# Kernel tuning notes

Measured on AMD Instinct MI355X. Metric: run time of the kernel, lower is better.

## Reference

```python
import jax, jax.numpy as jnp
import numpy as np

N_NODES = 50000
N_EDGES = 800000
F_IN = 128
F_HID = 128
N_CLS = 1
E_TR = 100000
E_TE = 20000


def setup_inputs() -> dict:
    key = jax.random.key(0)
    ks = jax.random.split(key, 16)
    inp = {
        'x': jax.random.normal(ks[0], (N_NODES, F_IN), dtype=jnp.float32),
        'edge_index': jax.random.randint(ks[1], (2, N_EDGES), 0, N_NODES, dtype=jnp.int32),
        'pos_edges_train': jax.random.randint(ks[2], (2, E_TR), 0, N_NODES, dtype=jnp.int32),
        'neg_edges_train': jax.random.randint(ks[3], (2, E_TR), 0, N_NODES, dtype=jnp.int32),
        'pos_edges_test': jax.random.randint(ks[4], (2, E_TE), 0, N_NODES, dtype=jnp.int32),
        'neg_edges_test': jax.random.randint(ks[5], (2, E_TE), 0, N_NODES, dtype=jnp.int32),
    }
    s = 0.05
    inp['W0'] = jax.random.normal(ks[6], (F_IN, F_HID), dtype=jnp.float32) * s
    inp['b0'] = jnp.zeros((F_HID,), dtype=jnp.float32)
    inp['W1'] = jax.random.normal(ks[7], (F_HID, F_HID), dtype=jnp.float32) * s
    inp['b1'] = jnp.zeros((F_HID,), dtype=jnp.float32)
    inp['W2'] = jax.random.normal(ks[8], (F_HID, F_HID), dtype=jnp.float32) * s
    inp['b2'] = jnp.zeros((F_HID,), dtype=jnp.float32)
    inp['W3'] = jax.random.normal(ks[9], (F_HID, F_HID), dtype=jnp.float32) * s
    inp['b3'] = jnp.zeros((F_HID,), dtype=jnp.float32)
    inp['Wl1'] = jax.random.normal(ks[10], (2 * F_HID, F_HID), dtype=jnp.float32) * s
    inp['bl1'] = jnp.zeros((F_HID,), dtype=jnp.float32)
    inp['Wl2'] = jax.random.normal(ks[11], (F_HID, N_CLS), dtype=jnp.float32) * s
    inp['bl2'] = jnp.zeros((N_CLS,), dtype=jnp.float32)
    return inp


def _gcn_conv(h, W, b, src, dst, dis):
    # PyG GCNConv: out = D^{-1/2}(A+I)D^{-1/2} (h W) + b, with self loops folded in analytically
    hw = h @ W                                           # [N, F]
    msg = hw[src] * dis[src][:, None]                    # [E, F]
    agg = jax.ops.segment_sum(msg, dst, num_segments=N_NODES)
    return agg * dis[:, None] + hw * (dis ** 2)[:, None] + b


def _edge_feats(x, e):
    return jnp.concatenate([x[e[0]], x[e[1]]], axis=1)


def reference(x, edge_index, pos_edges_train, neg_edges_train, pos_edges_test, neg_edges_test,
              W0, b0, W1, b1, W2, b2, W3, b3, Wl1, bl1, Wl2, bl2):
    src, dst = edge_index[0], edge_index[1]
    # degree with self loop (+1), symmetric normalization
    deg = jax.ops.segment_sum(jnp.ones((src.shape[0],), jnp.float32), dst, num_segments=N_NODES) + 1.0
    dis = deg ** -0.5

    h = jax.nn.relu(_gcn_conv(x, W0, b0, src, dst, dis))
    h = jax.nn.relu(_gcn_conv(h, W1, b1, src, dst, dis))
    h = jax.nn.relu(_gcn_conv(h, W2, b2, src, dst, dis))
    h = _gcn_conv(h, W3, b3, src, dst, dis)

    x_train = jnp.concatenate([_edge_feats(h, pos_edges_train), _edge_feats(h, neg_edges_train)], axis=0)
    x_test = jnp.concatenate([_edge_feats(h, pos_edges_test), _edge_feats(h, neg_edges_test)], axis=0)
    n_train = x_train.shape[0]
    z = jnp.concatenate([x_train, x_test], axis=0)
    z = jax.nn.relu(z @ Wl1 + bl1)
    z = (z @ Wl2 + bl2).squeeze(1)
    return (z[:n_train], z[n_train:])
```

## Files before the change

kernel.cpp:

```cpp
#include <hip/hip_runtime.h>
#include <math.h>

#define NN 50000
#define NE 800000
#define FD 128
#define SCAN_B 196
#define NTR 100000
#define NTE 20000


__global__ __launch_bounds__(256) void k_zero_int(int* __restrict__ p, int n) {
    int i = blockIdx.x * 256 + threadIdx.x;
    if (i < n) p[i] = 0;
}

__global__ __launch_bounds__(256) void k_count(const int* __restrict__ dst, int* __restrict__ deg) {
    int e = blockIdx.x * 256 + threadIdx.x;
    if (e < NE) atomicAdd(&deg[dst[e]], 1);
}


__global__ __launch_bounds__(256) void k_scan1(const int* __restrict__ deg,
                                               int* __restrict__ partial,
                                               int* __restrict__ bsum,
                                               float* __restrict__ dis) {
    __shared__ int wsum[4];
    const int t = threadIdx.x, lane = t & 63, wid = t >> 6;
    const int i = blockIdx.x * 256 + t;
    int v = (i < NN) ? deg[i] : 0;
    int sc = v;
#pragma unroll
    for (int d = 1; d < 64; d <<= 1) {
        int o = __shfl_up(sc, d, 64);
        if (lane >= d) sc += o;
    }
    if (lane == 63) wsum[wid] = sc;
    __syncthreads();
    int pre = 0;
    for (int w = 0; w < wid; ++w) pre += wsum[w];
    if (i < NN) {
        partial[i] = pre + sc - v;
        dis[i] = (float)(1.0 / sqrt((double)(v + 1)));
    }
    if (t == 255) bsum[blockIdx.x] = pre + sc;
}

__global__ __launch_bounds__(256) void k_scan2(int* __restrict__ bsum) {
    __shared__ int wsum[4];
    const int t = threadIdx.x, lane = t & 63, wid = t >> 6;
    int v = (t < SCAN_B) ? bsum[t] : 0;
    int sc = v;
#pragma unroll
    for (int d = 1; d < 64; d <<= 1) {
        int o = __shfl_up(sc, d, 64);
        if (lane >= d) sc += o;
    }
    if (lane == 63) wsum[wid] = sc;
    __syncthreads();
    int pre = 0;
    for (int w = 0; w < wid; ++w) pre += wsum[w];
    if (t < SCAN_B) bsum[t] = pre + sc - v;
}

__global__ __launch_bounds__(256) void k_scan3(const int* __restrict__ partial,
                                               const int* __restrict__ bsum,
                                               int* __restrict__ offs,
                                               int* __restrict__ cursor) {
    const int i = blockIdx.x * 256 + threadIdx.x;
    if (i < NN) {
        int o = partial[i] + bsum[blockIdx.x];
        offs[i] = o;
        cursor[i] = o;
    }
    if (i == 0) offs[NN] = NE;
}


__global__ __launch_bounds__(256) void k_fill(const int* __restrict__ src, const int* __restrict__ dst,
                                              int* __restrict__ cursor, int* __restrict__ srcs_sorted) {
    int e = blockIdx.x * 256 + threadIdx.x;
    if (e < NE) {
        int d = dst[e];
        int p = atomicAdd(&cursor[d], 1);
        srcs_sorted[p] = src[e];
    }
}


__global__ __launch_bounds__(256) void k_gemm(const float* __restrict__ A,
                                              const float* __restrict__ W,
                                              const float* __restrict__ dis,
                                              float* __restrict__ C, int nrows) {
    __shared__ float As[32][128];
    const int t = threadIdx.x;
    const int row0 = blockIdx.x * 32;

    for (int idx = t; idx < 32 * 32; idx += 256) {
        int r = idx >> 5, c = idx & 31;
        float4 v = make_float4(0.f, 0.f, 0.f, 0.f);
        if (row0 + r < nrows)
            v = reinterpret_cast<const float4*>(A)[(size_t)(row0 + r) * 32 + c];
        reinterpret_cast<float4*>(&As[r][0])[c] = v;
    }
    __syncthreads();

    const int cg = t & 31;
    const int eg = t >> 5;
    float acc[4][4] = {{0.f}};

    const float4* W4 = reinterpret_cast<const float4*>(W);
    const float4* As4 = reinterpret_cast<const float4*>(As);

    float4 w0 = W4[0 * 32 + cg];
    float4 w1 = W4[1 * 32 + cg];
    float4 w2 = W4[2 * 32 + cg];
    float4 w3 = W4[3 * 32 + cg];

    for (int k4 = 0; k4 < 32; ++k4) {
        int kn = (k4 < 31) ? (k4 + 1) : 31;
        float4 n0 = W4[(kn * 4 + 0) * 32 + cg];
        float4 n1 = W4[(kn * 4 + 1) * 32 + cg];
        float4 n2 = W4[(kn * 4 + 2) * 32 + cg];
        float4 n3 = W4[(kn * 4 + 3) * 32 + cg];
#pragma unroll
        for (int i = 0; i < 4; ++i) {
            float4 a = As4[(eg * 4 + i) * 32 + k4];
            acc[i][0] += a.x * w0.x + a.y * w1.x + a.z * w2.x + a.w * w3.x;
            acc[i][1] += a.x * w0.y + a.y * w1.y + a.z * w2.y + a.w * w3.y;
            acc[i][2] += a.x * w0.z + a.y * w1.z + a.z * w2.z + a.w * w3.z;
            acc[i][3] += a.x * w0.w + a.y * w1.w + a.z * w2.w + a.w * w3.w;
        }
        w0 = n0; w1 = n1; w2 = n2; w3 = n3;
    }

#pragma unroll
    for (int i = 0; i < 4; ++i) {
        int r = row0 + eg * 4 + i;
        if (r < nrows) {
            float d = dis[r];
            float4 o = make_float4(acc[i][0] * d, acc[i][1] * d, acc[i][2] * d, acc[i][3] * d);
            reinterpret_cast<float4*>(C)[(size_t)r * 32 + cg] = o;
        }
    }
}


__global__ __launch_bounds__(256) void k_fused_gg(const float* __restrict__ hws_in,
                                                  const float* __restrict__ dis,
                                                  const float* __restrict__ bprev,
                                                  const float* __restrict__ W,
                                                  const int* __restrict__ offs,
                                                  const int* __restrict__ srcs,
                                                  float* __restrict__ hws_out, int nrows) {
    __shared__ float As[32][128];
    const int t = threadIdx.x;
    const int f4 = t & 31;
    const int ng = t >> 5;
    const int row0 = blockIdx.x * 32;

    const float4* H4 = reinterpret_cast<const float4*>(hws_in);
    float4 bb = reinterpret_cast<const float4*>(bprev)[f4];

#pragma unroll
    for (int j = 0; j < 4; ++j) {
        int nl = ng * 4 + j;
        int node = row0 + nl;
        float4 o = make_float4(0.f, 0.f, 0.f, 0.f);
        if (node < nrows) {
            float4 acc = H4[(size_t)node * 32 + f4];
            const int e0 = offs[node], e1 = offs[node + 1];
            int e = e0;
            for (; e + 8 <= e1; e += 8) {
                int s0 = srcs[e + 0], s1 = srcs[e + 1], s2 = srcs[e + 2], s3 = srcs[e + 3];
                int s4 = srcs[e + 4], s5 = srcs[e + 5], s6 = srcs[e + 6], s7 = srcs[e + 7];
                float4 v0 = H4[(size_t)s0 * 32 + f4];
                float4 v1 = H4[(size_t)s1 * 32 + f4];
                float4 v2 = H4[(size_t)s2 * 32 + f4];
                float4 v3 = H4[(size_t)s3 * 32 + f4];
                float4 v4 = H4[(size_t)s4 * 32 + f4];
                float4 v5 = H4[(size_t)s5 * 32 + f4];
                float4 v6 = H4[(size_t)s6 * 32 + f4];
                float4 v7 = H4[(size_t)s7 * 32 + f4];
                acc.x += ((v0.x + v1.x) + (v2.x + v3.x)) + ((v4.x + v5.x) + (v6.x + v7.x));
                acc.y += ((v0.y + v1.y) + (v2.y + v3.y)) + ((v4.y + v5.y) + (v6.y + v7.y));
                acc.z += ((v0.z + v1.z) + (v2.z + v3.z)) + ((v4.z + v5.z) + (v6.z + v7.z));
                acc.w += ((v0.w + v1.w) + (v2.w + v3.w)) + ((v4.w + v5.w) + (v6.w + v7.w));
            }
            for (; e < e1; ++e) {
                int s = srcs[e];
                float4 v = H4[(size_t)s * 32 + f4];
                acc.x += v.x; acc.y += v.y; acc.z += v.z; acc.w += v.w;
            }
            float d = dis[node];
            o.x = fmaxf(acc.x * d + bb.x, 0.f);
            o.y = fmaxf(acc.y * d + bb.y, 0.f);
            o.z = fmaxf(acc.z * d + bb.z, 0.f);
            o.w = fmaxf(acc.w * d + bb.w, 0.f);
        }
        reinterpret_cast<float4*>(&As[nl][0])[f4] = o;
    }
    asm volatile("s_waitcnt lgkmcnt(0)" ::: "memory");

    const int cg = f4;
    const int eg = ng;
    float acc[4][4] = {{0.f}};

    const float4* W4 = reinterpret_cast<const float4*>(W);
    const float4* As4 = reinterpret_cast<const float4*>(As);

    float4 w0 = W4[0 * 32 + cg];
    float4 w1 = W4[1 * 32 + cg];
    float4 w2 = W4[2 * 32 + cg];
    float4 w3 = W4[3 * 32 + cg];

    for (int k4 = 0; k4 < 32; ++k4) {
        int kn = (k4 < 31) ? (k4 + 1) : 31;
        float4 n0 = W4[(kn * 4 + 0) * 32 + cg];
        float4 n1 = W4[(kn * 4 + 1) * 32 + cg];
        float4 n2 = W4[(kn * 4 + 2) * 32 + cg];
        float4 n3 = W4[(kn * 4 + 3) * 32 + cg];
#pragma unroll
        for (int i = 0; i < 4; ++i) {
            float4 a = As4[(eg * 4 + i) * 32 + k4];
            acc[i][0] += a.x * w0.x + a.y * w1.x + a.z * w2.x + a.w * w3.x;
            acc[i][1] += a.x * w0.y + a.y * w1.y + a.z * w2.y + a.w * w3.y;
            acc[i][2] += a.x * w0.z + a.y * w1.z + a.z * w2.z + a.w * w3.z;
            acc[i][3] += a.x * w0.w + a.y * w1.w + a.z * w2.w + a.w * w3.w;
        }
        w0 = n0; w1 = n1; w2 = n2; w3 = n3;
    }

#pragma unroll
    for (int i = 0; i < 4; ++i) {
        int r = row0 + eg * 4 + i;
        if (r < nrows) {
            float d = dis[r];
            float4 o = make_float4(acc[i][0] * d, acc[i][1] * d, acc[i][2] * d, acc[i][3] * d);
            reinterpret_cast<float4*>(hws_out)[(size_t)r * 32 + cg] = o;
        }
    }
}


__global__ __launch_bounds__(256) void k_fused_uv(const float* __restrict__ hws_in,
                                                  const float* __restrict__ dis,
                                                  const float* __restrict__ bprev,
                                                  const float* __restrict__ Wa,
                                                  const float* __restrict__ Wb,
                                                  const int* __restrict__ offs,
                                                  const int* __restrict__ srcs,
                                                  float* __restrict__ U,
                                                  float* __restrict__ V, int nrows) {
    __shared__ float As[32][128];
    const int t = threadIdx.x;
    const int f4 = t & 31;
    const int ng = t >> 5;
    const int row0 = blockIdx.x * 32;

    const float4* H4 = reinterpret_cast<const float4*>(hws_in);
    float4 bb = reinterpret_cast<const float4*>(bprev)[f4];

#pragma unroll
    for (int j = 0; j < 4; ++j) {
        int nl = ng * 4 + j;
        int node = row0 + nl;
        float4 o = make_float4(0.f, 0.f, 0.f, 0.f);
        if (node < nrows) {
            float4 acc = H4[(size_t)node * 32 + f4];
            const int e0 = offs[node], e1 = offs[node + 1];
            int e = e0;
            for (; e + 8 <= e1; e += 8) {
                int s0 = srcs[e + 0], s1 = srcs[e + 1], s2 = srcs[e + 2], s3 = srcs[e + 3];
                int s4 = srcs[e + 4], s5 = srcs[e + 5], s6 = srcs[e + 6], s7 = srcs[e + 7];
                float4 v0 = H4[(size_t)s0 * 32 + f4];
                float4 v1 = H4[(size_t)s1 * 32 + f4];
                float4 v2 = H4[(size_t)s2 * 32 + f4];
                float4 v3 = H4[(size_t)s3 * 32 + f4];
                float4 v4 = H4[(size_t)s4 * 32 + f4];
                float4 v5 = H4[(size_t)s5 * 32 + f4];
                float4 v6 = H4[(size_t)s6 * 32 + f4];
                float4 v7 = H4[(size_t)s7 * 32 + f4];
                acc.x += ((v0.x + v1.x) + (v2.x + v3.x)) + ((v4.x + v5.x) + (v6.x + v7.x));
                acc.y += ((v0.y + v1.y) + (v2.y + v3.y)) + ((v4.y + v5.y) + (v6.y + v7.y));
                acc.z += ((v0.z + v1.z) + (v2.z + v3.z)) + ((v4.z + v5.z) + (v6.z + v7.z));
                acc.w += ((v0.w + v1.w) + (v2.w + v3.w)) + ((v4.w + v5.w) + (v6.w + v7.w));
            }
            for (; e < e1; ++e) {
                int s = srcs[e];
                float4 v = H4[(size_t)s * 32 + f4];
                acc.x += v.x; acc.y += v.y; acc.z += v.z; acc.w += v.w;
            }
            float d = dis[node];
            o.x = acc.x * d + bb.x;
            o.y = acc.y * d + bb.y;
            o.z = acc.z * d + bb.z;
            o.w = acc.w * d + bb.w;
        }
        reinterpret_cast<float4*>(&As[nl][0])[f4] = o;
    }
    asm volatile("s_waitcnt lgkmcnt(0)" ::: "memory");

    const int cg = f4;
    const int eg = ng;
    const float4* As4 = reinterpret_cast<const float4*>(As);

#pragma unroll
    for (int pass = 0; pass < 2; ++pass) {
        const float4* W4 = reinterpret_cast<const float4*>(pass ? Wb : Wa);
        float* C = pass ? V : U;
        float acc[4][4] = {{0.f}};

        float4 w0 = W4[0 * 32 + cg];
        float4 w1 = W4[1 * 32 + cg];
        float4 w2 = W4[2 * 32 + cg];
        float4 w3 = W4[3 * 32 + cg];

        for (int k4 = 0; k4 < 32; ++k4) {
            int kn = (k4 < 31) ? (k4 + 1) : 31;
            float4 n0 = W4[(kn * 4 + 0) * 32 + cg];
            float4 n1 = W4[(kn * 4 + 1) * 32 + cg];
            float4 n2 = W4[(kn * 4 + 2) * 32 + cg];
            float4 n3 = W4[(kn * 4 + 3) * 32 + cg];
#pragma unroll
            for (int i = 0; i < 4; ++i) {
                float4 a = As4[(eg * 4 + i) * 32 + k4];
                acc[i][0] += a.x * w0.x + a.y * w1.x + a.z * w2.x + a.w * w3.x;
                acc[i][1] += a.x * w0.y + a.y * w1.y + a.z * w2.y + a.w * w3.y;
                acc[i][2] += a.x * w0.z + a.y * w1.z + a.z * w2.z + a.w * w3.z;
                acc[i][3] += a.x * w0.w + a.y * w1.w + a.z * w2.w + a.w * w3.w;
            }
            w0 = n0; w1 = n1; w2 = n2; w3 = n3;
        }

#pragma unroll
        for (int i = 0; i < 4; ++i) {
            int r = row0 + eg * 4 + i;
            if (r < nrows) {
                float4 o = make_float4(acc[i][0], acc[i][1], acc[i][2], acc[i][3]);
                reinterpret_cast<float4*>(C)[(size_t)r * 32 + cg] = o;
            }
        }
    }
}


__global__ __launch_bounds__(256) void k_edge_score(const float* __restrict__ U,
                                                    const float* __restrict__ V,
                                                    const int* __restrict__ tp,
                                                    const int* __restrict__ tn,
                                                    const int* __restrict__ sp,
                                                    const int* __restrict__ sn,
                                                    const float* __restrict__ bl1,
                                                    const float* __restrict__ Wl2,
                                                    const float* __restrict__ bl2,
                                                    float* __restrict__ out) {
    const int t = threadIdx.x;
    const int f4 = t & 31;
    const int e = blockIdx.x * 8 + (t >> 5);
    if (e >= 2 * NTR + 2 * NTE) return;

    int a, bn;
    if (e < NTR)                { a = tp[e];              bn = tp[e + NTR]; }
    else if (e < 2 * NTR)       { a = tn[e - NTR];        bn = tn[e]; }
    else if (e < 2 * NTR + NTE) { a = sp[e - 2 * NTR];    bn = sp[e - 2 * NTR + NTE]; }
    else                        { a = sn[e - 2 * NTR - NTE]; bn = sn[e - 2 * NTR]; }

    float4 u = reinterpret_cast<const float4*>(U)[(size_t)a * 32 + f4];
    float4 v = reinterpret_cast<const float4*>(V)[(size_t)bn * 32 + f4];
    float4 bb = reinterpret_cast<const float4*>(bl1)[f4];
    float4 w2 = reinterpret_cast<const float4*>(Wl2)[f4];

    float s = fmaxf(u.x + v.x + bb.x, 0.f) * w2.x
            + fmaxf(u.y + v.y + bb.y, 0.f) * w2.y
            + fmaxf(u.z + v.z + bb.z, 0.f) * w2.z
            + fmaxf(u.w + v.w + bb.w, 0.f) * w2.w;
#pragma unroll
    for (int m = 16; m >= 1; m >>= 1) s += __shfl_xor(s, m, 64);
    if (f4 == 0) out[e] = s + bl2[0];
}


extern "C" void kernel_launch(void* const* d_in, const int* in_sizes, int n_in,
                              void* d_out, int out_size, void* d_ws, size_t ws_size,
                              hipStream_t stream) {
    const float* x = (const float*)d_in[0];
    const int* ei = (const int*)d_in[1];
    const int* srcp = ei;
    const int* dstp = ei + NE;

    const int* e_tr_pos = (const int*)d_in[2];
    const int* e_tr_neg = (const int*)d_in[3];
    const int* e_te_pos = (const int*)d_in[4];
    const int* e_te_neg = (const int*)d_in[5];

    const float* W[4] = {(const float*)d_in[6], (const float*)d_in[8],
                         (const float*)d_in[10], (const float*)d_in[12]};
    const float* b[4] = {(const float*)d_in[7], (const float*)d_in[9],
                         (const float*)d_in[11], (const float*)d_in[13]};
    const float* Wl1 = (const float*)d_in[14];
    const float* bl1 = (const float*)d_in[15];
    const float* Wl2 = (const float*)d_in[16];
    const float* bl2 = (const float*)d_in[17];

    float* ws = (float*)d_ws;
    float* dis = ws;
    int* deg = (int*)(ws + 50176);
    int* offs = (int*)(ws + 100352);
    int* cursor = (int*)(ws + 150784);
    int* bsum = (int*)(ws + 200960);
    int* srcs = (int*)(ws + 201216);
    float* B0 = ws + 1001216;
    float* B1 = B0 + 6400000;
    float* B2 = B1 + 6400000;
    int* partial = (int*)B2;

    k_zero_int<<<(NN + 255) / 256, 256, 0, stream>>>(deg, NN);
    k_count<<<(NE + 255) / 256, 256, 0, stream>>>(dstp, deg);
    k_scan1<<<SCAN_B, 256, 0, stream>>>(deg, partial, bsum, dis);
    k_scan2<<<1, 256, 0, stream>>>(bsum);
    k_scan3<<<SCAN_B, 256, 0, stream>>>(partial, bsum, offs, cursor);
    k_fill<<<(NE + 255) / 256, 256, 0, stream>>>(srcp, dstp, cursor, srcs);

    const int gemm_blocks = (NN + 31) / 32;

    k_gemm<<<gemm_blocks, 256, 0, stream>>>(x, W[0], dis, B0, NN);
    k_fused_gg<<<gemm_blocks, 256, 0, stream>>>(B0, dis, b[0], W[1], offs, srcs, B1, NN);
    k_fused_gg<<<gemm_blocks, 256, 0, stream>>>(B1, dis, b[1], W[2], offs, srcs, B0, NN);
    k_fused_gg<<<gemm_blocks, 256, 0, stream>>>(B0, dis, b[2], W[3], offs, srcs, B1, NN);
    float* Ubuf = B0;
    float* Vbuf = B2;
    k_fused_uv<<<gemm_blocks, 256, 0, stream>>>(B1, dis, b[3], Wl1, Wl1 + 128 * 128,
                                                offs, srcs, Ubuf, Vbuf, NN);

    float* out = (float*)d_out;
    const int n_all = 2 * NTR + 2 * NTE;
    k_edge_score<<<(n_all + 7) / 8, 256, 0, stream>>>(Ubuf, Vbuf,
                                                      e_tr_pos, e_tr_neg, e_te_pos, e_te_neg,
                                                      bl1, Wl2, bl2, out);
}
```

Baseline: 535.6 us.

## Drop scan2 and zero kernels, merge UV passes, add wave priority hints

The separate block-sum scan kernel is removed: each scan3 block now reduces the preceding block sums itself. The degree-zeroing kernel is replaced by hipMemsetAsync. The two sequential GEMM passes in the fused UV kernel become one pass that accumulates U and V together, so each A tile is read from LDS once. s_setprio hints are placed around the GEMM inner loops. Together these aim to cut launch count and LDS traffic, at the cost of more registers in the UV kernel, which may lower occupancy.

```diff
diff --git a/kernel.cpp b/kernel.cpp
--- a/kernel.cpp
+++ b/kernel.cpp
@@ -8,11 +8,6 @@
 #define NTR 100000
 #define NTE 20000
 
-
-__global__ __launch_bounds__(256) void k_zero_int(int* __restrict__ p, int n) {
-    int i = blockIdx.x * 256 + threadIdx.x;
-    if (i < n) p[i] = 0;
-}
 
 __global__ __launch_bounds__(256) void k_count(const int* __restrict__ dst, int* __restrict__ deg) {
     int e = blockIdx.x * 256 + threadIdx.x;
@@ -45,34 +40,26 @@
     if (t == 255) bsum[blockIdx.x] = pre + sc;
 }
 
-__global__ __launch_bounds__(256) void k_scan2(int* __restrict__ bsum) {
-    __shared__ int wsum[4];
-    const int t = threadIdx.x, lane = t & 63, wid = t >> 6;
-    int v = (t < SCAN_B) ? bsum[t] : 0;
-    int sc = v;
-#pragma unroll
-    for (int d = 1; d < 64; d <<= 1) {
-        int o = __shfl_up(sc, d, 64);
-        if (lane >= d) sc += o;
-    }
-    if (lane == 63) wsum[wid] = sc;
-    __syncthreads();
-    int pre = 0;
-    for (int w = 0; w < wid; ++w) pre += wsum[w];
-    if (t < SCAN_B) bsum[t] = pre + sc - v;
-}
 
 __global__ __launch_bounds__(256) void k_scan3(const int* __restrict__ partial,
                                                const int* __restrict__ bsum,
                                                int* __restrict__ offs,
                                                int* __restrict__ cursor) {
-    const int i = blockIdx.x * 256 + threadIdx.x;
+    __shared__ int wsum[4];
+    const int t = threadIdx.x, lane = t & 63, wid = t >> 6;
+    int v = (t < blockIdx.x && t < SCAN_B) ? bsum[t] : 0;
+#pragma unroll
+    for (int m = 32; m >= 1; m >>= 1) v += __shfl_xor(v, m, 64);
+    if (lane == 0) wsum[wid] = v;
+    __syncthreads();
+    int pre = wsum[0] + wsum[1] + wsum[2] + wsum[3];
+    const int i = blockIdx.x * 256 + t;
     if (i < NN) {
-        int o = partial[i] + bsum[blockIdx.x];
+        int o = partial[i] + pre;
         offs[i] = o;
         cursor[i] = o;
     }
-    if (i == 0) offs[NN] = NE;
+    if (blockIdx.x == 0 && t == 0) offs[NN] = NE;
 }
 
 
@@ -213,6 +200,7 @@
     float4 w2 = W4[2 * 32 + cg];
     float4 w3 = W4[3 * 32 + cg];
 
+    __builtin_amdgcn_s_setprio(1);
     for (int k4 = 0; k4 < 32; ++k4) {
         int kn = (k4 < 31) ? (k4 + 1) : 31;
         float4 n0 = W4[(kn * 4 + 0) * 32 + cg];
@@ -229,6 +217,7 @@
         }
         w0 = n0; w1 = n1; w2 = n2; w3 = n3;
     }
+    __builtin_amdgcn_s_setprio(0);
 
 #pragma unroll
     for (int i = 0; i < 4; ++i) {
@@ -303,42 +292,45 @@
     const int cg = f4;
     const int eg = ng;
     const float4* As4 = reinterpret_cast<const float4*>(As);
-
-#pragma unroll
-    for (int pass = 0; pass < 2; ++pass) {
-        const float4* W4 = reinterpret_cast<const float4*>(pass ? Wb : Wa);
-        float* C = pass ? V : U;
-        float acc[4][4] = {{0.f}};
-
-        float4 w0 = W4[0 * 32 + cg];
-        float4 w1 = W4[1 * 32 + cg];
-        float4 w2 = W4[2 * 32 + cg];
-        float4 w3 = W4[3 * 32 + cg];
-
-        for (int k4 = 0; k4 < 32; ++k4) {
-            int kn = (k4 < 31) ? (k4 + 1) : 31;
-            float4 n0 = W4[(kn * 4 + 0) * 32 + cg];
-            float4 n1 = W4[(kn * 4 + 1) * 32 + cg];
-            float4 n2 = W4[(kn * 4 + 2) * 32 + cg];
-            float4 n3 = W4[(kn * 4 + 3) * 32 + cg];
-#pragma unroll
-            for (int i = 0; i < 4; ++i) {
-                float4 a = As4[(eg * 4 + i) * 32 + k4];
-                acc[i][0] += a.x * w0.x + a.y * w1.x + a.z * w2.x + a.w * w3.x;
-                acc[i][1] += a.x * w0.y + a.y * w1.y + a.z * w2.y + a.w * w3.y;
-                acc[i][2] += a.x * w0.z + a.y * w1.z + a.z * w2.z + a.w * w3.z;
-                acc[i][3] += a.x * w0.w + a.y * w1.w + a.z * w2.w + a.w * w3.w;
-            }
-            w0 = n0; w1 = n1; w2 = n2; w3 = n3;
-        }
-
+    const float4* Wa4 = reinterpret_cast<const float4*>(Wa);
+    const float4* Wb4 = reinterpret_cast<const float4*>(Wb);
+
+    float accU[4][4] = {{0.f}};
+    float accV[4][4] = {{0.f}};
+
+    __builtin_amdgcn_s_setprio(1);
+    for (int k4 = 0; k4 < 32; ++k4) {
+        float4 wa0 = Wa4[(k4 * 4 + 0) * 32 + cg];
+        float4 wa1 = Wa4[(k4 * 4 + 1) * 32 + cg];
+        float4 wa2 = Wa4[(k4 * 4 + 2) * 32 + cg];
+        float4 wa3 = Wa4[(k4 * 4 + 3) * 32 + cg];
+        float4 wb0 = Wb4[(k4 * 4 + 0) * 32 + cg];
+        float4 wb1 = Wb4[(k4 * 4 + 1) * 32 + cg];
+        float4 wb2 = Wb4[(k4 * 4 + 2) * 32 + cg];
+        float4 wb3 = Wb4[(k4 * 4 + 3) * 32 + cg];
 #pragma unroll
         for (int i = 0; i < 4; ++i) {
-            int r = row0 + eg * 4 + i;
-            if (r < nrows) {
-                float4 o = make_float4(acc[i][0], acc[i][1], acc[i][2], acc[i][3]);
-                reinterpret_cast<float4*>(C)[(size_t)r * 32 + cg] = o;
-            }
+            float4 a = As4[(eg * 4 + i) * 32 + k4];
+            accU[i][0] += a.x * wa0.x + a.y * wa1.x + a.z * wa2.x + a.w * wa3.x;
+            accU[i][1] += a.x * wa0.y + a.y * wa1.y + a.z * wa2.y + a.w * wa3.y;
+            accU[i][2] += a.x * wa0.z + a.y * wa1.z + a.z * wa2.z + a.w * wa3.z;
+            accU[i][3] += a.x * wa0.w + a.y * wa1.w + a.z * wa2.w + a.w * wa3.w;
+            accV[i][0] += a.x * wb0.x + a.y * wb1.x + a.z * wb2.x + a.w * wb3.x;
+            accV[i][1] += a.x * wb0.y + a.y * wb1.y + a.z * wb2.y + a.w * wb3.y;
+            accV[i][2] += a.x * wb0.z + a.y * wb1.z + a.z * wb2.z + a.w * wb3.z;
+            accV[i][3] += a.x * wb0.w + a.y * wb1.w + a.z * wb2.w + a.w * wb3.w;
+        }
+    }
+    __builtin_amdgcn_s_setprio(0);
+
+#pragma unroll
+    for (int i = 0; i < 4; ++i) {
+        int r = row0 + eg * 4 + i;
+        if (r < nrows) {
+            reinterpret_cast<float4*>(U)[(size_t)r * 32 + cg] =
+                make_float4(accU[i][0], accU[i][1], accU[i][2], accU[i][3]);
+            reinterpret_cast<float4*>(V)[(size_t)r * 32 + cg] =
+                make_float4(accV[i][0], accV[i][1], accV[i][2], accV[i][3]);
         }
     }
 }
@@ -414,10 +406,9 @@
     float* B2 = B1 + 6400000;
     int* partial = (int*)B2;
 
-    k_zero_int<<<(NN + 255) / 256, 256, 0, stream>>>(deg, NN);
+    hipMemsetAsync(deg, 0, NN * sizeof(int), stream);
     k_count<<<(NE + 255) / 256, 256, 0, stream>>>(dstp, deg);
     k_scan1<<<SCAN_B, 256, 0, stream>>>(deg, partial, bsum, dis);
-    k_scan2<<<1, 256, 0, stream>>>(bsum);
     k_scan3<<<SCAN_B, 256, 0, stream>>>(partial, bsum, offs, cursor);
     k_fill<<<(NE + 255) / 256, 256, 0, stream>>>(srcp, dstp, cursor, srcs);
 
```

Result: slower. 549.6 us (+2.6%).
